# Optimization experiments

Measured on AMD Instinct MI355X. Metric: run time of the kernel, lower is better.

## Reference

```python
import jax, jax.numpy as jnp
import numpy as np

HEADS = 16
DK = 64
THETA = 10000.0


def _rope(x, cos, sin):
    # x: (B, S, H, dk) -> rotate consecutive pairs as complex numbers
    xr = x.reshape(*x.shape[:-1], -1, 2)
    a, b = xr[..., 0], xr[..., 1]
    c = cos[None, :, None, :]  # (1, S, 1, dk//2)
    s = sin[None, :, None, :]
    out = jnp.stack([a * c - b * s, a * s + b * c], axis=-1)
    return out.reshape(x.shape)


def setup_inputs() -> dict:
    key = jax.random.key(0)
    ks = jax.random.split(key, 5)
    B, S, D = 4, 2048, 1024
    x = jax.random.normal(ks[0], (B, S, D), dtype=jnp.float32)
    scale = 1.0 / np.sqrt(D).astype(np.float32)
    Wq = jax.random.normal(ks[1], (D, D), dtype=jnp.float32) * scale
    Wk = jax.random.normal(ks[2], (D, D), dtype=jnp.float32) * scale
    Wv = jax.random.normal(ks[3], (D, D), dtype=jnp.float32) * scale
    Wo = jax.random.normal(ks[4], (D, D), dtype=jnp.float32) * scale
    # freqs_cis = exp(i * t * theta^{-2j/dk}), represented as cos/sin
    t = jnp.arange(S, dtype=jnp.float32)
    inv_freq = 1.0 / (THETA ** (jnp.arange(0, DK, 2, dtype=jnp.float32) / DK))
    ang = t[:, None] * inv_freq[None, :]  # (S, dk//2)
    return {"in_features": x, "freqs_cos": jnp.cos(ang), "freqs_sin": jnp.sin(ang),
            "Wq": Wq, "Wk": Wk, "Wv": Wv, "Wo": Wo}


def reference(in_features, freqs_cos, freqs_sin, Wq, Wk, Wv, Wo):
    B, S, D = in_features.shape
    H = HEADS
    dk = D // H
    # Linear projections (torch Linear: x @ W.T)
    q = (in_features @ Wq.T).reshape(B, S, H, dk)
    k = (in_features @ Wk.T).reshape(B, S, H, dk)
    v = (in_features @ Wv.T).reshape(B, S, H, dk)
    q = _rope(q, freqs_cos, freqs_sin)
    k = _rope(k, freqs_cos, freqs_sin)
    scale = 1.0 / jnp.sqrt(jnp.asarray(dk, dtype=q.dtype))
    scores = jnp.einsum("bqhd,bkhd->bhqk", q, k) * scale
    mask = jnp.tril(jnp.ones((S, S), dtype=bool))
    scores = jnp.where(mask[None, None, :, :], scores, -jnp.inf)
    attn = jax.nn.softmax(scores, axis=-1)
    out = jnp.einsum("bhqk,bkhd->bqhd", attn, v).reshape(B, S, D)
    return out @ Wo.T
```

## Files before the change

### kernel.cpp

```cpp
#include <hip/hip_runtime.h>
#include <hip/hip_bf16.h>

typedef __attribute__((ext_vector_type(8))) __bf16 bf16x8;
typedef __attribute__((ext_vector_type(4))) __bf16 bf16x4;
typedef __attribute__((ext_vector_type(4))) float f32x4;
typedef __attribute__((ext_vector_type(2))) unsigned int u32x2;

static __device__ __forceinline__ f32x4 mfma_bf16(bf16x8 a, bf16x8 b, f32x4 c) {
  return __builtin_amdgcn_mfma_f32_16x16x32_bf16(a, b, c, 0, 0, 0);
}

static __device__ __forceinline__ void gload_lds16(const void* g, void* l) {
  __builtin_amdgcn_global_load_lds(
      (__attribute__((address_space(1))) unsigned int*)g,
      (__attribute__((address_space(3))) unsigned int*)l, 16, 0, 0);
}

static __device__ __forceinline__ unsigned int pk_bf16(float a, float b) {
  union { __bf16 h; unsigned short u; } x, y;
  x.h = (__bf16)a; y.h = (__bf16)b;
  return ((unsigned int)y.u << 16) | x.u;
}

__global__ void cvt_bf16(const float* __restrict__ in, __bf16* __restrict__ out, int n4) {
  int i = blockIdx.x * blockDim.x + threadIdx.x;
  if (i >= n4) return;
  f32x4 v = ((const f32x4*)in)[i];
  bf16x4 o;
#pragma unroll
  for (int k = 0; k < 4; ++k) o[k] = (__bf16)v[k];
  ((bf16x4*)out)[i] = o;
}

template <int MODE>
__global__ __launch_bounds__(512, 1)
void gemm256(const __bf16* __restrict__ A, const __bf16* __restrict__ W,
             void* __restrict__ outp,
             const float* __restrict__ fcos, const float* __restrict__ fsin) {
  constexpr int K = 1024;
  constexpr int NT = K / 64;
  extern __shared__ __align__(16) __bf16 dynlds[];
  __bf16* Al = dynlds;
  __bf16* Bl = dynlds + 49152;

  const int t = threadIdx.x;
  const int lane = t & 63, wave = t >> 6;
  const int g = lane >> 4, ln = lane & 15;
  const int wm = wave >> 2, wn = wave & 3;
  const int bn = blockIdx.x, bm = blockIdx.y;

  f32x4 acc[8][2] = {};

  const int srow8 = t >> 3;
  const int scole = (((t & 7) ^ ((t >> 3) & 7)) << 3);
  const __bf16* Ag = A + (size_t)(bm * 256 + srow8) * K + scole;
  const __bf16* Wg = W + (size_t)(bn * 128 + srow8) * K + scole;

#define ISSUE_A(kt, slot)                                                   \
  {                                                                         \
    const int k0 = (kt) * 64;                                               \
    __bf16* d = Al + (slot) * 16384 + t * 8;                                \
    gload_lds16(Ag + k0, d);                                                \
    gload_lds16(Ag + (size_t)64 * K + k0, d + 4096);                        \
    gload_lds16(Ag + (size_t)128 * K + k0, d + 8192);                       \
    gload_lds16(Ag + (size_t)192 * K + k0, d + 12288);                      \
  }
#define ISSUE_B(kt, slot)                                                   \
  {                                                                         \
    const int k0 = (kt) * 64;                                               \
    __bf16* d = Bl + (slot) * 8192 + t * 8;                                 \
    gload_lds16(Wg + k0, d);                                                \
    gload_lds16(Wg + (size_t)64 * K + k0, d + 4096);                        \
  }

  const int axr = ln & 7;
  int aoff[8], boff[2];
#pragma unroll
  for (int i = 0; i < 8; ++i) aoff[i] = (wm * 128 + i * 16 + ln) * 64;
#pragma unroll
  for (int j = 0; j < 2; ++j) boff[j] = (wn * 32 + j * 16 + ln) * 64;

  ISSUE_A(0, 0);
  ISSUE_B(0, 0);
  ISSUE_A(1, 1);

#define TILE_BODY(tt, LAST)                                                 \
  {                                                                         \
    if (LAST) { asm volatile("s_waitcnt vmcnt(0)" ::: "memory"); }          \
    else      { asm volatile("s_waitcnt vmcnt(4)" ::: "memory"); }          \
    __builtin_amdgcn_s_barrier();                                           \
    __builtin_amdgcn_sched_barrier(0);                                      \
    const __bf16* Ab = Al + ((tt) % 3) * 16384;                             \
    const __bf16* Bb = Bl + ((tt) & 1) * 8192;                              \
    bf16x8 af[8], bf[2];                                                    \
                                                               \
    _Pragma("unroll") for (int i = 0; i < 8; ++i)                           \
      af[i] = *(const bf16x8*)(Ab + aoff[i] + ((g ^ axr) << 3));            \
    _Pragma("unroll") for (int j = 0; j < 2; ++j)                           \
      bf[j] = *(const bf16x8*)(Bb + boff[j] + ((g ^ axr) << 3));            \
    if (!(LAST)) ISSUE_B((tt) + 1, ((tt) + 1) & 1);                         \
    __builtin_amdgcn_s_setprio(1);                                          \
    _Pragma("unroll") for (int i = 0; i < 8; ++i)                           \
      _Pragma("unroll") for (int j = 0; j < 2; ++j)                         \
        acc[i][j] = mfma_bf16(af[i], bf[j], acc[i][j]);                     \
    __builtin_amdgcn_s_setprio(0);                                          \
                                                               \
    _Pragma("unroll") for (int i = 0; i < 8; ++i)                           \
      af[i] = *(const bf16x8*)(Ab + aoff[i] + (((4 | g) ^ axr) << 3));      \
    _Pragma("unroll") for (int j = 0; j < 2; ++j)                           \
      bf[j] = *(const bf16x8*)(Bb + boff[j] + (((4 | g) ^ axr) << 3));      \
    if ((tt) + 2 < NT) ISSUE_A((tt) + 2, ((tt) + 2) % 3);                   \
    __builtin_amdgcn_s_setprio(1);                                          \
    _Pragma("unroll") for (int i = 0; i < 8; ++i)                           \
      _Pragma("unroll") for (int j = 0; j < 2; ++j)                         \
        acc[i][j] = mfma_bf16(af[i], bf[j], acc[i][j]);                     \
    __builtin_amdgcn_s_setprio(0);                                          \
  }

  for (int tt = 0; tt < NT - 1; ++tt) TILE_BODY(tt, false);
  TILE_BODY(NT - 1, true);
#undef TILE_BODY
#undef ISSUE_A
#undef ISSUE_B

#pragma unroll
  for (int i = 0; i < 8; ++i) {
    const int mbase = bm * 256 + wm * 128 + i * 16 + g * 4;
#pragma unroll
    for (int j = 0; j < 2; ++j) {
      const int col = bn * 128 + wn * 32 + j * 16 + ln;
      if constexpr (MODE == 0 || MODE == 1) {
        const int fi = (col & 63) >> 1;
        const bool odd = (col & 1) != 0;
        __bf16* O = (__bf16*)outp;
#pragma unroll
        for (int r = 0; r < 4; ++r) {
          const int row = mbase + r;
          const int tok = row & 2047;
          const float cs = fcos[tok * 32 + fi];
          const float sn = fsin[tok * 32 + fi];
          const float own = acc[i][j][r];
          const float oth = __shfl_xor(own, 1);
          float val = own * cs + (odd ? oth * sn : -oth * sn);
          if constexpr (MODE == 0) val *= 0.1803368802f;
          O[(size_t)row * 1024 + col] = (__bf16)val;
        }
      } else if constexpr (MODE == 2) {
        __bf16* O = (__bf16*)outp;
        const int bb = mbase >> 11;
        const int tok = mbase & 2047;
        bf16x4 pk;
#pragma unroll
        for (int r = 0; r < 4; ++r) pk[r] = (__bf16)acc[i][j][r];
        *(bf16x4*)(O + ((size_t)(bb * 1024 + col)) * 2048 + tok) = pk;
      } else {
        float* O = (float*)outp;
#pragma unroll
        for (int r = 0; r < 4; ++r)
          O[(size_t)(mbase + r) * 1024 + col] = acc[i][j][r];
      }
    }
  }
}

__global__ __launch_bounds__(512, 4)
void attn_fwd(const __bf16* __restrict__ Q, const __bf16* __restrict__ Kk,
              const __bf16* __restrict__ Vt, __bf16* __restrict__ U) {
  constexpr int S = 2048;
  __shared__ __align__(16) __bf16 Klds[2][2 * 64 * 32];
  __shared__ __align__(16) __bf16 Vlds[2][2 * 64 * 32];
  __shared__ __align__(16) unsigned int Plds[8][16 * 36];

  const int t = threadIdx.x;
  const int lane = t & 63, wave = t >> 6;
  const int g = lane >> 4, ln = lane & 15;
  const int qt = blockIdx.x;
  const int bh = blockIdx.y;
  const int b = bh >> 4, h = bh & 15;
  const int q0s[2] = {qt * 128, (15 - qt) * 128};
  const int nts[2] = {2 * qt + 2, 32 - 2 * qt};

  bf16x8 qf[2][2];
#pragma unroll
  for (int s2 = 0; s2 < 2; ++s2) {
    const __bf16* Qb = Q + ((size_t)(b * S + q0s[s2] + wave * 16 + ln)) * 1024 + h * 64;
    qf[s2][0] = *(const bf16x8*)(Qb + g * 8);
    qf[s2][1] = *(const bf16x8*)(Qb + 32 + g * 8);
  }

  f32x4 o[2][4] = {};
  float mrow[2], lrow[2];
#pragma unroll
  for (int s2 = 0; s2 < 2; ++s2) { mrow[s2] = -3.0e38f; lrow[s2] = 0.f; }

  const int half = t >> 8;
  const int srow = (t >> 2) & 63;
  const int scol = (t & 3) * 8;
  const __bf16* Kg = Kk + ((size_t)(b * S + srow)) * 1024 + h * 64 + half * 32 + scol;
  const __bf16* Vg = Vt + ((size_t)(b * 1024 + h * 64 + srow)) * 2048 + half * 32 + scol;
  const int nt = nts[1];

  gload_lds16(Kg, (__bf16*)Klds[0] + t * 8);
  gload_lds16(Vg, (__bf16*)Vlds[0] + t * 8);
  __syncthreads();

  for (int kt = 0; kt < nt; ++kt) {
    const int cur = kt & 1;
    if (kt + 1 < nt) {
      const size_t kv1 = (size_t)(kt + 1) * 64;
      gload_lds16(Kg + kv1 * 1024, (__bf16*)Klds[cur ^ 1] + t * 8);
      gload_lds16(Vg + kv1, (__bf16*)Vlds[cur ^ 1] + t * 8);
    }
    const int kv0 = kt * 64;

#pragma unroll
    for (int s2 = 0; s2 < 2; ++s2) {
      if (kt >= nts[s2]) continue;

      f32x4 sa[4] = {};
      __builtin_amdgcn_s_setprio(1);
#pragma unroll
      for (int s = 0; s < 2; ++s) {
#pragma unroll
        for (int c = 0; c < 4; ++c) {
          bf16x8 kf = *(const bf16x8*)(Klds[cur] + s * 2048 + (c * 16 + ln) * 32 + g * 8);
          sa[c] = mfma_bf16(kf, qf[s2][s], sa[c]);
        }
      }
      __builtin_amdgcn_s_setprio(0);

      const int rfbase = q0s[s2] + wave * 16;
      const int rq = rfbase + ln;
      if (kv0 + 63 > rfbase) {
#pragma unroll
        for (int c = 0; c < 4; ++c)
#pragma unroll
          for (int r = 0; r < 4; ++r)
            if (kv0 + c * 16 + g * 4 + r > rq) sa[c][r] = -1e30f;
      }

      float tm[8];
#pragma unroll
      for (int i = 0; i < 8; ++i) tm[i] = fmaxf(sa[i >> 2][i & 3], sa[2 + (i >> 2)][i & 3]);
#pragma unroll
      for (int st = 4; st >= 1; st >>= 1)
#pragma unroll
        for (int i = 0; i < st; ++i) tm[i] = fmaxf(tm[i], tm[i + st]);
      float pm = tm[0];

      if (__any(pm > mrow[s2] + 8.f)) {
        pm = fmaxf(pm, __shfl_xor(pm, 16));
        pm = fmaxf(pm, __shfl_xor(pm, 32));
        const float mn = fmaxf(mrow[s2], pm);
        const float alpha = exp2f(mrow[s2] - mn);
        mrow[s2] = mn;
        lrow[s2] *= alpha;
#pragma unroll
        for (int c2 = 0; c2 < 4; ++c2)
#pragma unroll
          for (int r = 0; r < 4; ++r) o[s2][c2][r] *= alpha;
      }

      float p[4][4];
#pragma unroll
      for (int c = 0; c < 4; ++c)
#pragma unroll
        for (int r = 0; r < 4; ++r) p[c][r] = exp2f(sa[c][r] - mrow[s2]);

      float ts[8];
#pragma unroll
      for (int i = 0; i < 8; ++i) ts[i] = p[i >> 2][i & 3] + p[2 + (i >> 2)][i & 3];
#pragma unroll
      for (int st = 4; st >= 1; st >>= 1)
#pragma unroll
        for (int i = 0; i < st; ++i) ts[i] += ts[i + st];
      float rs = ts[0];
      rs += __shfl_xor(rs, 16);
      rs += __shfl_xor(rs, 32);
      lrow[s2] += rs;

      unsigned int* Pw = Plds[wave] + ln * 36;
#pragma unroll
      for (int c = 0; c < 4; ++c) {
        u32x2 w;
        w[0] = pk_bf16(p[c][0], p[c][1]);
        w[1] = pk_bf16(p[c][2], p[c][3]);
        *(u32x2*)(Pw + 8 * c + 2 * g) = w;
      }

      __builtin_amdgcn_s_setprio(1);
#pragma unroll
      for (int sh = 0; sh < 2; ++sh) {
        bf16x8 pb = *(const bf16x8*)((const __bf16*)(Plds[wave]) + ln * 72 + sh * 32 + g * 8);
#pragma unroll
        for (int c2 = 0; c2 < 4; ++c2) {
          bf16x8 vf = *(const bf16x8*)(Vlds[cur] + sh * 2048 + (c2 * 16 + ln) * 32 + g * 8);
          o[s2][c2] = mfma_bf16(vf, pb, o[s2][c2]);
        }
      }
      __builtin_amdgcn_s_setprio(0);
    }
    __syncthreads();
  }

#pragma unroll
  for (int s2 = 0; s2 < 2; ++s2) {
    const float rl = 1.0f / lrow[s2];
    __bf16* Ub = U + ((size_t)(b * S + q0s[s2] + wave * 16 + ln)) * 1024 + h * 64;
#pragma unroll
    for (int c2 = 0; c2 < 4; ++c2) {
      bf16x4 pk4;
#pragma unroll
      for (int r = 0; r < 4; ++r) pk4[r] = (__bf16)(o[s2][c2][r] * rl);
      *(bf16x4*)(Ub + 16 * c2 + 4 * g) = pk4;
    }
  }
}

extern "C" void kernel_launch(void* const* d_in, const int* in_sizes, int n_in,
                              void* d_out, int out_size, void* d_ws, size_t ws_size,
                              hipStream_t stream) {
  const float* x    = (const float*)d_in[0];
  const float* fcos = (const float*)d_in[1];
  const float* fsin = (const float*)d_in[2];
  const float* Wq   = (const float*)d_in[3];
  const float* Wk   = (const float*)d_in[4];
  const float* Wv   = (const float*)d_in[5];
  const float* Wo   = (const float*)d_in[6];

  char* ws = (char*)d_ws;
  __bf16* xb  = (__bf16*)(ws);
  __bf16* Wqb = (__bf16*)(ws + (16u << 20));
  __bf16* Wkb = (__bf16*)(ws + (18u << 20));
  __bf16* Wvb = (__bf16*)(ws + (20u << 20));
  __bf16* Wob = (__bf16*)(ws + (22u << 20));
  __bf16* Qb  = (__bf16*)(ws + (24u << 20));
  __bf16* Kb  = (__bf16*)(ws + (40u << 20));
  __bf16* Vtb = (__bf16*)(ws + (56u << 20));
  __bf16* Ub  = xb;

  cvt_bf16<<<8192, 256, 0, stream>>>(x,  xb,  8192 * 1024 / 4);
  cvt_bf16<<<1024, 256, 0, stream>>>(Wq, Wqb, 1024 * 1024 / 4);
  cvt_bf16<<<1024, 256, 0, stream>>>(Wk, Wkb, 1024 * 1024 / 4);
  cvt_bf16<<<1024, 256, 0, stream>>>(Wv, Wvb, 1024 * 1024 / 4);
  cvt_bf16<<<1024, 256, 0, stream>>>(Wo, Wob, 1024 * 1024 / 4);

  dim3 gg(8, 32);
  const size_t lds = 131072;
  gemm256<0><<<gg, 512, lds, stream>>>(xb, Wqb, Qb,  fcos, fsin);
  gemm256<1><<<gg, 512, lds, stream>>>(xb, Wkb, Kb,  fcos, fsin);
  gemm256<2><<<gg, 512, lds, stream>>>(xb, Wvb, Vtb, nullptr, nullptr);
  attn_fwd<<<dim3(8, 64), 512, 0, stream>>>(Qb, Kb, Vtb, Ub);
  gemm256<3><<<gg, 512, lds, stream>>>(Ub, Wob, d_out, nullptr, nullptr);
}
```

Baseline: 216.9 us.

## Reshape GEMM wave tiling to 4x4 and restructure pipeline; merge weight conversions

Changes the per-wave GEMM tile from 128x32 to 64x64, which raises MFMA operand reuse per LDS fragment load (8 loads per 16 MFMAs instead of 10). The k-loop is rewritten as a regular loop with a rotating slot index and extra barriers and lgkmcnt waits around each half-tile. The four weight conversion launches are merged into one grid with blockIdx.y selecting the matrix, removing launch overhead. The extra barriers per half-tile may add synchronization cost that offsets the reuse gain.

```diff
diff --git a/kernel.cpp b/kernel.cpp
--- a/kernel.cpp
+++ b/kernel.cpp
@@ -25,6 +25,25 @@
 __global__ void cvt_bf16(const float* __restrict__ in, __bf16* __restrict__ out, int n4) {
   int i = blockIdx.x * blockDim.x + threadIdx.x;
   if (i >= n4) return;
+  f32x4 v = ((const f32x4*)in)[i];
+  bf16x4 o;
+#pragma unroll
+  for (int k = 0; k < 4; ++k) o[k] = (__bf16)v[k];
+  ((bf16x4*)out)[i] = o;
+}
+
+__global__ void cvt_w4(const float* __restrict__ w0, const float* __restrict__ w1,
+                       const float* __restrict__ w2, const float* __restrict__ w3,
+                       __bf16* __restrict__ o0, __bf16* __restrict__ o1,
+                       __bf16* __restrict__ o2, __bf16* __restrict__ o3) {
+  const float* in; __bf16* out;
+  switch (blockIdx.y) {
+    case 0: in = w0; out = o0; break;
+    case 1: in = w1; out = o1; break;
+    case 2: in = w2; out = o2; break;
+    default: in = w3; out = o3; break;
+  }
+  int i = blockIdx.x * blockDim.x + threadIdx.x;
   f32x4 v = ((const f32x4*)in)[i];
   bf16x4 o;
 #pragma unroll
@@ -46,10 +65,10 @@
   const int t = threadIdx.x;
   const int lane = t & 63, wave = t >> 6;
   const int g = lane >> 4, ln = lane & 15;
-  const int wm = wave >> 2, wn = wave & 3;
+  const int wm = wave >> 1, wn = wave & 1;
   const int bn = blockIdx.x, bm = blockIdx.y;
 
-  f32x4 acc[8][2] = {};
+  f32x4 acc[4][4] = {};
 
   const int srow8 = t >> 3;
   const int scole = (((t & 7) ^ ((t >> 3) & 7)) << 3);
@@ -74,61 +93,75 @@
   }
 
   const int axr = ln & 7;
-  int aoff[8], boff[2];
-#pragma unroll
-  for (int i = 0; i < 8; ++i) aoff[i] = (wm * 128 + i * 16 + ln) * 64;
-#pragma unroll
-  for (int j = 0; j < 2; ++j) boff[j] = (wn * 32 + j * 16 + ln) * 64;
-
+  int aoff[4], boff[4];
+#pragma unroll
+  for (int i = 0; i < 4; ++i) aoff[i] = (wm * 64 + i * 16 + ln) * 64;
+#pragma unroll
+  for (int j = 0; j < 4; ++j) boff[j] = (wn * 64 + j * 16 + ln) * 64;
+
+  ISSUE_B(0, 0);
   ISSUE_A(0, 0);
-  ISSUE_B(0, 0);
   ISSUE_A(1, 1);
-
-#define TILE_BODY(tt, LAST)                                                 \
-  {                                                                         \
-    if (LAST) { asm volatile("s_waitcnt vmcnt(0)" ::: "memory"); }          \
-    else      { asm volatile("s_waitcnt vmcnt(4)" ::: "memory"); }          \
-    __builtin_amdgcn_s_barrier();                                           \
-    __builtin_amdgcn_sched_barrier(0);                                      \
-    const __bf16* Ab = Al + ((tt) % 3) * 16384;                             \
-    const __bf16* Bb = Bl + ((tt) & 1) * 8192;                              \
-    bf16x8 af[8], bf[2];                                                    \
-                                                               \
-    _Pragma("unroll") for (int i = 0; i < 8; ++i)                           \
-      af[i] = *(const bf16x8*)(Ab + aoff[i] + ((g ^ axr) << 3));            \
-    _Pragma("unroll") for (int j = 0; j < 2; ++j)                           \
-      bf[j] = *(const bf16x8*)(Bb + boff[j] + ((g ^ axr) << 3));            \
-    if (!(LAST)) ISSUE_B((tt) + 1, ((tt) + 1) & 1);                         \
-    __builtin_amdgcn_s_setprio(1);                                          \
-    _Pragma("unroll") for (int i = 0; i < 8; ++i)                           \
-      _Pragma("unroll") for (int j = 0; j < 2; ++j)                         \
-        acc[i][j] = mfma_bf16(af[i], bf[j], acc[i][j]);                     \
-    __builtin_amdgcn_s_setprio(0);                                          \
-                                                               \
-    _Pragma("unroll") for (int i = 0; i < 8; ++i)                           \
-      af[i] = *(const bf16x8*)(Ab + aoff[i] + (((4 | g) ^ axr) << 3));      \
-    _Pragma("unroll") for (int j = 0; j < 2; ++j)                           \
-      bf[j] = *(const bf16x8*)(Bb + boff[j] + (((4 | g) ^ axr) << 3));      \
-    if ((tt) + 2 < NT) ISSUE_A((tt) + 2, ((tt) + 2) % 3);                   \
-    __builtin_amdgcn_s_setprio(1);                                          \
-    _Pragma("unroll") for (int i = 0; i < 8; ++i)                           \
-      _Pragma("unroll") for (int j = 0; j < 2; ++j)                         \
-        acc[i][j] = mfma_bf16(af[i], bf[j], acc[i][j]);                     \
-    __builtin_amdgcn_s_setprio(0);                                          \
-  }
-
-  for (int tt = 0; tt < NT - 1; ++tt) TILE_BODY(tt, false);
-  TILE_BODY(NT - 1, true);
-#undef TILE_BODY
+  asm volatile("s_waitcnt vmcnt(4)" ::: "memory");
+  __builtin_amdgcn_s_barrier();
+
+  int sa = 0;
+  for (int tt = 0; tt < NT; ++tt) {
+    const __bf16* Ab = Al + sa * 16384;
+    const __bf16* Bb = Bl + (tt & 1) * 8192;
+    bf16x8 af[4], bf[4];
+
+#pragma unroll
+    for (int i = 0; i < 4; ++i)
+      af[i] = *(const bf16x8*)(Ab + aoff[i] + ((g ^ axr) << 3));
+#pragma unroll
+    for (int j = 0; j < 4; ++j)
+      bf[j] = *(const bf16x8*)(Bb + boff[j] + ((g ^ axr) << 3));
+    if (tt + 1 < NT) ISSUE_B(tt + 1, (tt + 1) & 1);
+    if (tt + 2 < NT) ISSUE_A(tt + 2, sa == 0 ? 2 : sa - 1);
+    __builtin_amdgcn_s_barrier();
+    asm volatile("s_waitcnt lgkmcnt(0)" ::: "memory");
+    __builtin_amdgcn_sched_barrier(0);
+    __builtin_amdgcn_s_setprio(1);
+#pragma unroll
+    for (int i = 0; i < 4; ++i)
+#pragma unroll
+      for (int j = 0; j < 4; ++j)
+        acc[i][j] = mfma_bf16(af[i], bf[j], acc[i][j]);
+    __builtin_amdgcn_s_setprio(0);
+    __builtin_amdgcn_s_barrier();
+
+#pragma unroll
+    for (int i = 0; i < 4; ++i)
+      af[i] = *(const bf16x8*)(Ab + aoff[i] + (((4 | g) ^ axr) << 3));
+#pragma unroll
+    for (int j = 0; j < 4; ++j)
+      bf[j] = *(const bf16x8*)(Bb + boff[j] + (((4 | g) ^ axr) << 3));
+    if (tt < NT - 2) { asm volatile("s_waitcnt vmcnt(4)" ::: "memory"); }
+    else             { asm volatile("s_waitcnt vmcnt(0)" ::: "memory"); }
+    __builtin_amdgcn_s_barrier();
+    asm volatile("s_waitcnt lgkmcnt(0)" ::: "memory");
+    __builtin_amdgcn_sched_barrier(0);
+    __builtin_amdgcn_s_setprio(1);
+#pragma unroll
+    for (int i = 0; i < 4; ++i)
+#pragma unroll
+      for (int j = 0; j < 4; ++j)
+        acc[i][j] = mfma_bf16(af[i], bf[j], acc[i][j]);
+    __builtin_amdgcn_s_setprio(0);
+    __builtin_amdgcn_s_barrier();
+
+    sa = (sa == 2) ? 0 : sa + 1;
+  }
 #undef ISSUE_A
 #undef ISSUE_B
 
 #pragma unroll
-  for (int i = 0; i < 8; ++i) {
-    const int mbase = bm * 256 + wm * 128 + i * 16 + g * 4;
-#pragma unroll
-    for (int j = 0; j < 2; ++j) {
-      const int col = bn * 128 + wn * 32 + j * 16 + ln;
+  for (int i = 0; i < 4; ++i) {
+    const int mbase = bm * 256 + wm * 64 + i * 16 + g * 4;
+#pragma unroll
+    for (int j = 0; j < 4; ++j) {
+      const int col = bn * 128 + wn * 64 + j * 16 + ln;
       if constexpr (MODE == 0 || MODE == 1) {
         const int fi = (col & 63) >> 1;
         const bool odd = (col & 1) != 0;
@@ -339,11 +372,8 @@
   __bf16* Vtb = (__bf16*)(ws + (56u << 20));
   __bf16* Ub  = xb;
 
-  cvt_bf16<<<8192, 256, 0, stream>>>(x,  xb,  8192 * 1024 / 4);
-  cvt_bf16<<<1024, 256, 0, stream>>>(Wq, Wqb, 1024 * 1024 / 4);
-  cvt_bf16<<<1024, 256, 0, stream>>>(Wk, Wkb, 1024 * 1024 / 4);
-  cvt_bf16<<<1024, 256, 0, stream>>>(Wv, Wvb, 1024 * 1024 / 4);
-  cvt_bf16<<<1024, 256, 0, stream>>>(Wo, Wob, 1024 * 1024 / 4);
+  cvt_bf16<<<8192, 256, 0, stream>>>(x, xb, 8192 * 1024 / 4);
+  cvt_w4<<<dim3(1024, 4), 256, 0, stream>>>(Wq, Wk, Wv, Wo, Wqb, Wkb, Wvb, Wob);
 
   dim3 gg(8, 32);
   const size_t lds = 131072;
```

Result: faster. 210.5 us (-2.9%).
